# Optimization experiments

Measured on AMD Instinct MI355X. Metric: run time of the kernel, lower is better.

Reference implementation:

```python
import jax, jax.numpy as jnp
import numpy as np

N = 1048576   # collocation points
D_IN = 2      # PDE spatial dim
H = 256       # mlp_x hidden
R0 = R1 = R2 = 64  # Tucker ranks (mlp_quad_last_shape)
NQ0 = NQ1 = 1024   # quadrature points per axis (quad_concat)
HQ = 128      # mlp_quad hidden
HC = 128      # core_mlp hidden
C_IN = 64     # core_init feature dim


def _mlp(x, W1, b1, W2, b2):
    # 2-layer MLP with tanh, standing in for the torch nn.Sequential MLPs
    return jnp.tanh(x @ W1 + b1) @ W2 + b2


def _r_func(quad_x, eq_param):
    # quadrature weight per point, shape (n_i, 1)
    return jnp.sin(jnp.pi * eq_param[0] * quad_x)


def setup_inputs() -> dict:
    key = jax.random.key(0)
    ks = jax.random.split(key, 16)

    def rn(k, shape, fan_in):
        return jax.random.normal(k, shape, dtype=jnp.float32) / np.float32(np.sqrt(fan_in))

    return {
        "input": jax.random.normal(ks[0], (N, D_IN), dtype=jnp.float32),
        "eq_param": jnp.ones((1,), jnp.float32),
        "quad_x0": jax.random.uniform(ks[1], (NQ0, 1), dtype=jnp.float32),
        "quad_x1": jax.random.uniform(ks[2], (NQ1, 1), dtype=jnp.float32),
        "core_init": jax.random.normal(ks[3], (1, C_IN), dtype=jnp.float32),
        # mlp_x: D_IN -> H -> R0
        "Wx1": rn(ks[4], (D_IN, H), D_IN), "bx1": jnp.zeros((H,), jnp.float32),
        "Wx2": rn(ks[5], (H, R0), H), "bx2": jnp.zeros((R0,), jnp.float32),
        # mlp_quad[0]: 1 -> HQ -> R1
        "Wq01": rn(ks[6], (1, HQ), 1), "bq01": jnp.zeros((HQ,), jnp.float32),
        "Wq02": rn(ks[7], (HQ, R1), HQ), "bq02": jnp.zeros((R1,), jnp.float32),
        # mlp_quad[1]: 1 -> HQ -> R2
        "Wq11": rn(ks[8], (1, HQ), 1), "bq11": jnp.zeros((HQ,), jnp.float32),
        "Wq12": rn(ks[9], (HQ, R2), HQ), "bq12": jnp.zeros((R2,), jnp.float32),
        # core_mlp: C_IN -> HC -> R0*R1*R2
        "Wc1": rn(ks[10], (C_IN, HC), C_IN), "bc1": jnp.zeros((HC,), jnp.float32),
        "Wc2": rn(ks[11], (HC, R0 * R1 * R2), HC), "bc2": jnp.zeros((R0 * R1 * R2,), jnp.float32),
    }


def reference(input, eq_param, quad_x0, quad_x1, core_init,
              Wx1, bx1, Wx2, bx2,
              Wq01, bq01, Wq02, bq02,
              Wq11, bq11, Wq12, bq12,
              Wc1, bc1, Wc2, bc2):
    # y, m = r_func(quad_x, eq_param) -> per-axis quadrature weights (n_i, 1)
    y0 = _r_func(quad_x0, eq_param)
    y1 = _r_func(quad_x1, eq_param)

    lhs = _mlp(input, Wx1, bx1, Wx2, bx2)                 # (N, R0)
    core = _mlp(core_init, Wc1, bc1, Wc2, bc2)            # (1, R0*R1*R2)
    core = core.reshape(R0, R1, R2)

    # loop axis 0: movedim(1,0) -> (R1,R0,R2), contract R1, sum quad points
    core = jnp.moveaxis(core, 1, 0)
    oq0 = y0 * _mlp(quad_x0, Wq01, bq01, Wq02, bq02)      # (NQ0, R1)
    # einsum('x...,cx->c...') then sum over c, fused:
    core = jnp.einsum('xab,cx->ab', core, oq0)            # (R0, R2)

    # loop axis 1: movedim(1,0) -> (R2,R0), contract R2, sum quad points
    core = jnp.moveaxis(core, 1, 0)
    oq1 = y1 * _mlp(quad_x1, Wq11, bq11, Wq12, bq12)      # (NQ1, R2)
    core = jnp.einsum('xa,cx->a', core, oq1)              # (R0,)

    # out = lhs @ core_out.T  (core_out is 1D -> vector output)
    return lhs @ core                                      # (N,)
```

## Files before the change

kernel.cpp:

```cpp
#include <hip/hip_runtime.h>
#include <hip/hip_bf16.h>
#include <stdint.h>

#define NPTS   1048576
#define HID    256
#define NQ     1024
#define HQ     128
#define HC     128
#define CIN    64
#define CORE_N 262144


#define TWO_LOG2E 2.885390081777927f

__device__ __forceinline__ bool sniff_bf16(const void* eq) {
    return ((const uint16_t*)eq)[0] == 0x3F80u;
}

__device__ __forceinline__ float ldv(const void* p, int i, bool b16) {
    return b16 ? __bfloat162float(((const __hip_bfloat16*)p)[i])
               : ((const float*)p)[i];
}

__device__ __forceinline__ float fast_tanh(float x) {
    float e = __builtin_amdgcn_exp2f(x * TWO_LOG2E);
    float r = __builtin_amdgcn_rcpf(e + 1.0f);
    return fmaf(-2.0f, r, 1.0f);
}

__global__ __launch_bounds__(1024) void k_small(
    const void* __restrict__ eq_param,
    const void* __restrict__ qx0, const void* __restrict__ qx1,
    const void* __restrict__ Wq01, const void* __restrict__ bq01,
    const void* __restrict__ Wq02, const void* __restrict__ bq02,
    const void* __restrict__ Wq11, const void* __restrict__ bq11,
    const void* __restrict__ Wq12, const void* __restrict__ bq12,
    const void* __restrict__ core_init,
    const void* __restrict__ Wc1, const void* __restrict__ bc1,
    float* __restrict__ ws)
{
    bool b16 = sniff_bf16(eq_param);
    int tid = threadIdx.x;
    int blk = blockIdx.x;
    if (blk == 2) {
        if (tid < HC) {
            float acc = ldv(bc1, tid, b16);
            for (int i = 0; i < CIN; ++i)
                acc = fmaf(ldv(core_init, i, b16), ldv(Wc1, i * HC + tid, b16), acc);
            ws[128 + tid] = fast_tanh(acc);
        } else if (tid < HC + 64) {
            ws[256 + (tid - HC) * 32] = 0.0f;
        }
        return;
    }
    const void* qx = blk ? qx1 : qx0;
    const void* W1 = blk ? Wq11 : Wq01;
    const void* b1 = blk ? bq11 : bq01;
    const void* W2 = blk ? Wq12 : Wq02;
    const void* b2 = blk ? bq12 : bq02;

    __shared__ float upart[8][HQ];
    __shared__ float ypart[8];
    __shared__ float uj[HQ];
    __shared__ float Ytot;

    int j = tid & 127;
    int cs = tid >> 7;
    float w1 = ldv(W1, j, b16), b1j = ldv(b1, j, b16);
    float eq = ldv(eq_param, 0, b16);
    const float PI = 3.14159265358979323846f;

    float u = 0.f, ysum = 0.f;
    for (int c = cs * 128; c < cs * 128 + 128; ++c) {
        float q = ldv(qx, c, b16);
        float y = __sinf(PI * eq * q);
        ysum += y;
        u += y * fast_tanh(fmaf(q, w1, b1j));
    }
    upart[cs][j] = u;
    if (j == 0) ypart[cs] = ysum;
    __syncthreads();
    if (tid < HQ) {
        float s = 0.f;
        for (int k = 0; k < 8; ++k) s += upart[k][tid];
        uj[tid] = s;
        if (tid == 0) { float Y = 0.f; for (int k = 0; k < 8; ++k) Y += ypart[k]; Ytot = Y; }
    }
    __syncthreads();
    if (tid < 64) {
        float s = Ytot * ldv(b2, tid, b16);
        for (int jj = 0; jj < HQ; ++jj) s = fmaf(uj[jj], ldv(W2, jj * 64 + tid, b16), s);
        ws[blk * 64 + tid] = s;
    }
}

__device__ __forceinline__ float chunk_dot_bf16(
    const uint4* __restrict__ rp, int lane,
    const float* __restrict__ s0v, const float* __restrict__ s1v)
{
    float acc = 0.f;
    #pragma unroll
    for (int kk = 0; kk < 8; ++kk) {
        uint4 v = rp[kk * 64 + lane];
        uint32_t uu[4] = {v.x, v.y, v.z, v.w};
        float inner = 0.f;
        #pragma unroll
        for (int q = 0; q < 4; ++q) {
            float lo = __uint_as_float(uu[q] << 16);
            float hi = __uint_as_float(uu[q] & 0xffff0000u);
            inner = fmaf(lo, s1v[2 * q], inner);
            inner = fmaf(hi, s1v[2 * q + 1], inner);
        }
        acc = fmaf(inner, s0v[kk], acc);
    }
    return acc;
}

__device__ __forceinline__ float chunk_dot_f32(
    const float4* __restrict__ rp, int lane,
    const float* __restrict__ s0v, const float* __restrict__ s1v)
{
    float acc = 0.f;
    #pragma unroll
    for (int kk = 0; kk < 16; ++kk) {
        float4 v = rp[kk * 64 + lane];
        float inner = v.x * s1v[0];
        inner = fmaf(v.y, s1v[1], inner);
        inner = fmaf(v.z, s1v[2], inner);
        inner = fmaf(v.w, s1v[3], inner);
        acc = fmaf(inner, s0v[kk], acc);
    }
    return acc;
}

__global__ __launch_bounds__(256) void k_core(
    const void* __restrict__ Wc2, const void* __restrict__ bc2,
    const void* __restrict__ eq_param,
    const float* __restrict__ ws, float* __restrict__ cacc)
{
    bool b16 = sniff_bf16(eq_param);
    int tid = threadIdx.x;
    int lane = tid & 63;
    int W = blockIdx.x * 4 + (tid >> 6);
    int a = W & 63;
    int j0 = W >> 6;

    float acc = 0.f;
    if (b16) {
        int g = lane >> 3, yb = (lane & 7) * 8;
        float s1v[8], s0v[8];
        #pragma unroll
        for (int e = 0; e < 8; ++e) s1v[e] = ws[64 + yb + e];
        #pragma unroll
        for (int kk = 0; kk < 8; ++kk) s0v[kk] = ws[kk * 8 + g];

        const uint4* base = (const uint4*)((const __hip_bfloat16*)Wc2 + (size_t)a * 4096);
        const size_t rowstep = CORE_N / 8;
        #pragma unroll 2
        for (int k = 0; k < 4; ++k) {
            int j = j0 + 32 * k;
            float d = chunk_dot_bf16(base + (size_t)j * rowstep, lane, s0v, s1v);
            acc = fmaf(d, ws[128 + j], acc);
        }
        if (W < 64)
            acc += chunk_dot_bf16((const uint4*)((const __hip_bfloat16*)bc2 + (size_t)a * 4096),
                                  lane, s0v, s1v);
    } else {
        int g = lane >> 4, yb = (lane & 15) * 4;
        float s1v[4], s0v[16];
        #pragma unroll
        for (int e = 0; e < 4; ++e) s1v[e] = ws[64 + yb + e];
        #pragma unroll
        for (int kk = 0; kk < 16; ++kk) s0v[kk] = ws[kk * 4 + g];

        const float4* base = (const float4*)((const float*)Wc2 + (size_t)a * 4096);
        const size_t rowstep = CORE_N / 4;
        for (int k = 0; k < 4; ++k) {
            int j = j0 + 32 * k;
            float d = chunk_dot_f32(base + (size_t)j * rowstep, lane, s0v, s1v);
            acc = fmaf(d, ws[128 + j], acc);
        }
        if (W < 64)
            acc += chunk_dot_f32((const float4*)((const float*)bc2 + (size_t)a * 4096),
                                 lane, s0v, s1v);
    }

    for (int offl = 32; offl > 0; offl >>= 1) acc += __shfl_down(acc, offl);
    if (lane == 0) atomicAdd(&cacc[a * 32], acc);
}

__global__ __launch_bounds__(256) void k_prep(
    const void* __restrict__ Wx1, const void* __restrict__ bx1,
    const void* __restrict__ Wx2, const void* __restrict__ bx2,
    const void* __restrict__ eq_param,
    const float* __restrict__ cacc, float* __restrict__ ws)
{
    bool b16 = sniff_bf16(eq_param);
    __shared__ float cv[64];
    __shared__ float red[4];
    int tid = threadIdx.x;
    if (tid < 64) cv[tid] = cacc[tid * 32];
    __syncthreads();
    float w = 0.f;
    for (int a = 0; a < 64; ++a) w = fmaf(ldv(Wx2, tid * 64 + a, b16), cv[a], w);
    float4 t;
    t.x = TWO_LOG2E * ldv(Wx1, tid, b16);
    t.y = TWO_LOG2E * ldv(Wx1, HID + tid, b16);
    t.z = TWO_LOG2E * ldv(bx1, tid, b16);
    t.w = -2.0f * w;
    ((float4*)(ws + 2560))[tid] = t;

    float p = w + ((tid < 64) ? ldv(bx2, tid, b16) * cv[tid] : 0.f);
    for (int offl = 32; offl > 0; offl >>= 1) p += __shfl_down(p, offl);
    if ((tid & 63) == 0) red[tid >> 6] = p;
    __syncthreads();
    if (tid == 0) ws[3584] = red[0] + red[1] + red[2] + red[3];
}

__global__ __launch_bounds__(256) void k_main(
    const void* __restrict__ x, const void* __restrict__ eq_param,
    const float* __restrict__ ws, void* __restrict__ out)
{
    bool b16 = sniff_bf16(eq_param);
    const float4* __restrict__ tbl = (const float4*)(ws + 2560);
    const int stride = NPTS / 2;
    int p0 = blockIdx.x * 256 + threadIdx.x;

    float x0[2], x1[2], acc[2];
    if (b16) {
        #pragma unroll
        for (int i = 0; i < 2; ++i) {
            uint32_t u = ((const uint32_t*)x)[p0 + i * stride];
            x0[i] = __uint_as_float(u << 16);
            x1[i] = __uint_as_float(u & 0xffff0000u);
        }
    } else {
        #pragma unroll
        for (int i = 0; i < 2; ++i) {
            float2 v = ((const float2*)x)[p0 + i * stride];
            x0[i] = v.x;
            x1[i] = v.y;
        }
    }
    float boff = ws[3584];
    acc[0] = boff; acc[1] = boff;

    #pragma unroll 4
    for (int jj = 0; jj < HID; ++jj) {
        float4 t = tbl[jj];
        float g0 = fmaf(x0[0], t.x, fmaf(x1[0], t.y, t.z));
        float g1 = fmaf(x0[1], t.x, fmaf(x1[1], t.y, t.z));
        g0 = __builtin_fminf(g0, 30.0f);
        g1 = __builtin_fminf(g1, 30.0f);
        float A = __builtin_amdgcn_exp2f(g0) + 1.0f;
        float B = __builtin_amdgcn_exp2f(g1) + 1.0f;
        float rP = __builtin_amdgcn_rcpf(A * B);
        acc[0] = fmaf(t.w, B * rP, acc[0]);
        acc[1] = fmaf(t.w, A * rP, acc[1]);
    }
    if (b16) {
        #pragma unroll
        for (int i = 0; i < 2; ++i)
            ((__hip_bfloat16*)out)[p0 + i * stride] = __float2bfloat16(acc[i]);
    } else {
        #pragma unroll
        for (int i = 0; i < 2; ++i)
            ((float*)out)[p0 + i * stride] = acc[i];
    }
}

extern "C" void kernel_launch(void* const* d_in, const int* in_sizes, int n_in,
                              void* d_out, int out_size, void* d_ws, size_t ws_size,
                              hipStream_t stream) {
    (void)in_sizes; (void)n_in; (void)out_size; (void)ws_size;
    const void* input     = d_in[0];
    const void* eq_param  = d_in[1];
    const void* quad_x0   = d_in[2];
    const void* quad_x1   = d_in[3];
    const void* core_init = d_in[4];
    const void* Wx1  = d_in[5];
    const void* bx1  = d_in[6];
    const void* Wx2  = d_in[7];
    const void* bx2  = d_in[8];
    const void* Wq01 = d_in[9];
    const void* bq01 = d_in[10];
    const void* Wq02 = d_in[11];
    const void* bq02 = d_in[12];
    const void* Wq11 = d_in[13];
    const void* bq11 = d_in[14];
    const void* Wq12 = d_in[15];
    const void* bq12 = d_in[16];
    const void* Wc1  = d_in[17];
    const void* bc1  = d_in[18];
    const void* Wc2  = d_in[19];
    const void* bc2  = d_in[20];

    float* ws = (float*)d_ws;

    k_small<<<3, 1024, 0, stream>>>(eq_param, quad_x0, quad_x1,
                                    Wq01, bq01, Wq02, bq02,
                                    Wq11, bq11, Wq12, bq12,
                                    core_init, Wc1, bc1, ws);
    k_core<<<512, 256, 0, stream>>>(Wc2, bc2, eq_param, ws, ws + 256);
    k_prep<<<1, 256, 0, stream>>>(Wx1, bx1, Wx2, bx2, eq_param, ws + 256, ws);
    k_main<<<NPTS / 512, 256, 0, stream>>>(input, eq_param, ws, d_out);
}
```

Before: 352.4 us.

## Process four points per thread with packed float2 math; widen core-contraction grid

k_main now handles four points per thread instead of two. It uses 2-wide vector float arithmetic so the compiler can emit packed FMA/add/mul instructions, and shares one reciprocal per pair of points. This cuts VALU instruction count and table loads per point, at the cost of more registers and half as many blocks. k_core doubles its grid so each wave handles two weight chunks instead of four. It also switches to nontemporal vector loads for the large Wc2 stream, which adds parallelism for the memory-bound core reduction.

New measurement: 339.7 us, median of 2. 3.6% less time.

```diff
diff --git a/kernel.cpp b/kernel.cpp
--- a/kernel.cpp
+++ b/kernel.cpp
@@ -12,6 +12,10 @@
 
 
 #define TWO_LOG2E 2.885390081777927f
+
+typedef float    v2f  __attribute__((ext_vector_type(2)));
+typedef uint32_t u32x4 __attribute__((ext_vector_type(4)));
+typedef float    f32x4 __attribute__((ext_vector_type(4)));
 
 __device__ __forceinline__ bool sniff_bf16(const void* eq) {
     return ((const uint16_t*)eq)[0] == 0x3F80u;
@@ -95,19 +99,18 @@
 }
 
 __device__ __forceinline__ float chunk_dot_bf16(
-    const uint4* __restrict__ rp, int lane,
+    const u32x4* __restrict__ rp, int lane,
     const float* __restrict__ s0v, const float* __restrict__ s1v)
 {
     float acc = 0.f;
     #pragma unroll
     for (int kk = 0; kk < 8; ++kk) {
-        uint4 v = rp[kk * 64 + lane];
-        uint32_t uu[4] = {v.x, v.y, v.z, v.w};
+        u32x4 v = __builtin_nontemporal_load(rp + kk * 64 + lane);
         float inner = 0.f;
         #pragma unroll
         for (int q = 0; q < 4; ++q) {
-            float lo = __uint_as_float(uu[q] << 16);
-            float hi = __uint_as_float(uu[q] & 0xffff0000u);
+            float lo = __uint_as_float(v[q] << 16);
+            float hi = __uint_as_float(v[q] & 0xffff0000u);
             inner = fmaf(lo, s1v[2 * q], inner);
             inner = fmaf(hi, s1v[2 * q + 1], inner);
         }
@@ -117,17 +120,17 @@
 }
 
 __device__ __forceinline__ float chunk_dot_f32(
-    const float4* __restrict__ rp, int lane,
+    const f32x4* __restrict__ rp, int lane,
     const float* __restrict__ s0v, const float* __restrict__ s1v)
 {
     float acc = 0.f;
     #pragma unroll
     for (int kk = 0; kk < 16; ++kk) {
-        float4 v = rp[kk * 64 + lane];
-        float inner = v.x * s1v[0];
-        inner = fmaf(v.y, s1v[1], inner);
-        inner = fmaf(v.z, s1v[2], inner);
-        inner = fmaf(v.w, s1v[3], inner);
+        f32x4 v = __builtin_nontemporal_load(rp + kk * 64 + lane);
+        float inner = v[0] * s1v[0];
+        inner = fmaf(v[1], s1v[1], inner);
+        inner = fmaf(v[2], s1v[2], inner);
+        inner = fmaf(v[3], s1v[3], inner);
         acc = fmaf(inner, s0v[kk], acc);
     }
     return acc;
@@ -154,16 +157,16 @@
         #pragma unroll
         for (int kk = 0; kk < 8; ++kk) s0v[kk] = ws[kk * 8 + g];
 
-        const uint4* base = (const uint4*)((const __hip_bfloat16*)Wc2 + (size_t)a * 4096);
+        const u32x4* base = (const u32x4*)((const __hip_bfloat16*)Wc2 + (size_t)a * 4096);
         const size_t rowstep = CORE_N / 8;
-        #pragma unroll 2
-        for (int k = 0; k < 4; ++k) {
-            int j = j0 + 32 * k;
+        #pragma unroll
+        for (int k = 0; k < 2; ++k) {
+            int j = j0 + 64 * k;
             float d = chunk_dot_bf16(base + (size_t)j * rowstep, lane, s0v, s1v);
             acc = fmaf(d, ws[128 + j], acc);
         }
         if (W < 64)
-            acc += chunk_dot_bf16((const uint4*)((const __hip_bfloat16*)bc2 + (size_t)a * 4096),
+            acc += chunk_dot_bf16((const u32x4*)((const __hip_bfloat16*)bc2 + (size_t)a * 4096),
                                   lane, s0v, s1v);
     } else {
         int g = lane >> 4, yb = (lane & 15) * 4;
@@ -173,15 +176,16 @@
         #pragma unroll
         for (int kk = 0; kk < 16; ++kk) s0v[kk] = ws[kk * 4 + g];
 
-        const float4* base = (const float4*)((const float*)Wc2 + (size_t)a * 4096);
+        const f32x4* base = (const f32x4*)((const float*)Wc2 + (size_t)a * 4096);
         const size_t rowstep = CORE_N / 4;
-        for (int k = 0; k < 4; ++k) {
-            int j = j0 + 32 * k;
+        #pragma unroll
+        for (int k = 0; k < 2; ++k) {
+            int j = j0 + 64 * k;
             float d = chunk_dot_f32(base + (size_t)j * rowstep, lane, s0v, s1v);
             acc = fmaf(d, ws[128 + j], acc);
         }
         if (W < 64)
-            acc += chunk_dot_f32((const float4*)((const float*)bc2 + (size_t)a * 4096),
+            acc += chunk_dot_f32((const f32x4*)((const float*)bc2 + (size_t)a * 4096),
                                  lane, s0v, s1v);
     }
 
@@ -223,48 +227,59 @@
 {
     bool b16 = sniff_bf16(eq_param);
     const float4* __restrict__ tbl = (const float4*)(ws + 2560);
-    const int stride = NPTS / 2;
+    const int stride = NPTS / 4;
     int p0 = blockIdx.x * 256 + threadIdx.x;
 
-    float x0[2], x1[2], acc[2];
+    float x0[4], x1[4];
     if (b16) {
         #pragma unroll
-        for (int i = 0; i < 2; ++i) {
+        for (int i = 0; i < 4; ++i) {
             uint32_t u = ((const uint32_t*)x)[p0 + i * stride];
             x0[i] = __uint_as_float(u << 16);
             x1[i] = __uint_as_float(u & 0xffff0000u);
         }
     } else {
         #pragma unroll
-        for (int i = 0; i < 2; ++i) {
+        for (int i = 0; i < 4; ++i) {
             float2 v = ((const float2*)x)[p0 + i * stride];
             x0[i] = v.x;
             x1[i] = v.y;
         }
     }
+    v2f x0a = {x0[0], x0[1]}, x0b = {x0[2], x0[3]};
+    v2f x1a = {x1[0], x1[1]}, x1b = {x1[2], x1[3]};
+
     float boff = ws[3584];
-    acc[0] = boff; acc[1] = boff;
+    v2f acca = {boff, boff}, accb = {boff, boff};
 
     #pragma unroll 4
     for (int jj = 0; jj < HID; ++jj) {
         float4 t = tbl[jj];
-        float g0 = fmaf(x0[0], t.x, fmaf(x1[0], t.y, t.z));
-        float g1 = fmaf(x0[1], t.x, fmaf(x1[1], t.y, t.z));
-        g0 = __builtin_fminf(g0, 30.0f);
-        g1 = __builtin_fminf(g1, 30.0f);
-        float A = __builtin_amdgcn_exp2f(g0) + 1.0f;
-        float B = __builtin_amdgcn_exp2f(g1) + 1.0f;
-        float rP = __builtin_amdgcn_rcpf(A * B);
-        acc[0] = fmaf(t.w, B * rP, acc[0]);
-        acc[1] = fmaf(t.w, A * rP, acc[1]);
-    }
+        v2f txv = {t.x, t.x}, tyv = {t.y, t.y}, tzv = {t.z, t.z}, twv = {t.w, t.w};
+        v2f ga = x0a * txv + x1a * tyv + tzv;
+        v2f gb = x0b * txv + x1b * tyv + tzv;
+        ga.x = __builtin_fminf(ga.x, 30.0f); ga.y = __builtin_fminf(ga.y, 30.0f);
+        gb.x = __builtin_fminf(gb.x, 30.0f); gb.y = __builtin_fminf(gb.y, 30.0f);
+        v2f ea, eb;
+        ea.x = __builtin_amdgcn_exp2f(ga.x); ea.y = __builtin_amdgcn_exp2f(ga.y);
+        eb.x = __builtin_amdgcn_exp2f(gb.x); eb.y = __builtin_amdgcn_exp2f(gb.y);
+        v2f onev = {1.0f, 1.0f};
+        v2f Aa = ea + onev;
+        v2f Ab = eb + onev;
+        v2f R = Aa * Ab;
+        v2f r;
+        r.x = __builtin_amdgcn_rcpf(R.x); r.y = __builtin_amdgcn_rcpf(R.y);
+        acca = twv * (Ab * r) + acca;
+        accb = twv * (Aa * r) + accb;
+    }
+    float acc[4] = {acca.x, acca.y, accb.x, accb.y};
     if (b16) {
         #pragma unroll
-        for (int i = 0; i < 2; ++i)
+        for (int i = 0; i < 4; ++i)
             ((__hip_bfloat16*)out)[p0 + i * stride] = __float2bfloat16(acc[i]);
     } else {
         #pragma unroll
-        for (int i = 0; i < 2; ++i)
+        for (int i = 0; i < 4; ++i)
             ((float*)out)[p0 + i * stride] = acc[i];
     }
 }
@@ -301,7 +316,7 @@
                                     Wq01, bq01, Wq02, bq02,
                                     Wq11, bq11, Wq12, bq12,
                                     core_init, Wc1, bc1, ws);
-    k_core<<<512, 256, 0, stream>>>(Wc2, bc2, eq_param, ws, ws + 256);
+    k_core<<<1024, 256, 0, stream>>>(Wc2, bc2, eq_param, ws, ws + 256);
     k_prep<<<1, 256, 0, stream>>>(Wx1, bx1, Wx2, bx2, eq_param, ws + 256, ws);
-    k_main<<<NPTS / 512, 256, 0, stream>>>(input, eq_param, ws, d_out);
-}
+    k_main<<<NPTS / 1024, 256, 0, stream>>>(input, eq_param, ws, d_out);
+}
```
